# Performance work log

Hardware: AMD Instinct MI355X
Metric: run time of the kernel (lower is better)

Reference implementation:

```python
import jax, jax.numpy as jnp
import numpy as np

B, C, H, W = 4, 256, 48, 48
HEADS, DH = 8, 32
INNER = HEADS * DH
HID = 128  # max(16, INNER//2)
SCALE = DH ** -0.5
EPS = 1e-6


def setup_inputs() -> dict:
    key = jax.random.key(0)
    ks = jax.random.split(key, 32)
    s = 0.02
    inp = {
        'x': jax.random.normal(ks[0], (B, C, H, W), jnp.float32),
        'rgb_input': jax.random.uniform(ks[1], (B, 3, H, W), jnp.float32),
        'wq': jax.random.normal(ks[2], (INNER, C), jnp.float32) * s,
        'bq': jnp.zeros((INNER,), jnp.float32),
        'wk': jax.random.normal(ks[3], (INNER, C), jnp.float32) * s,
        'bk': jnp.zeros((INNER,), jnp.float32),
        'wv': jax.random.normal(ks[4], (INNER, C), jnp.float32) * s,
        'bv': jnp.zeros((INNER,), jnp.float32),
        'wproj': jax.random.normal(ks[5], (C, INNER), jnp.float32) * s,
        'bproj': jnp.zeros((C,), jnp.float32),
        'c1_w': jax.random.normal(ks[6], (HID, 1, 3, 3), jnp.float32) * s,
        'c1_b': jnp.zeros((HID,), jnp.float32),
        'c2_w': jax.random.normal(ks[7], (HID, HID, 3, 3), jnp.float32) * s,
        'c2_b': jnp.zeros((HID,), jnp.float32),
        'gq_w': jax.random.normal(ks[8], (INNER, HID), jnp.float32) * s,
        'gq_b': jnp.ones((INNER,), jnp.float32),
        'bqf_w': jax.random.normal(ks[9], (INNER, HID), jnp.float32) * s,
        'bqf_b': jnp.zeros((INNER,), jnp.float32),
        'gk_w': jax.random.normal(ks[10], (INNER, HID), jnp.float32) * s,
        'gk_b': jnp.ones((INNER,), jnp.float32),
        'bkf_w': jax.random.normal(ks[11], (INNER, HID), jnp.float32) * s,
        'bkf_b': jnp.zeros((INNER,), jnp.float32),
        'gv_w': jax.random.normal(ks[12], (INNER, HID), jnp.float32) * s,
        'gv_b': jnp.ones((INNER,), jnp.float32),
        'bvf_w': jax.random.normal(ks[13], (INNER, HID), jnp.float32) * s,
        'bvf_b': jnp.zeros((INNER,), jnp.float32),
        'alpha': jnp.float32(0.1),
    }
    return inp


def _conv3(x, w, b):
    y = jax.lax.conv_general_dilated(x, w, (1, 1), 'SAME',
                                     dimension_numbers=('NCHW', 'OIHW', 'NCHW'))
    return y + b[None, :, None, None]


def _rgb_to_luma(rgb):
    y = 0.299 * rgb[:, 0:1] + 0.587 * rgb[:, 1:2] + 0.114 * rgb[:, 2:3]
    y_min = jnp.min(y, axis=(2, 3), keepdims=True)
    y_max = jnp.max(y, axis=(2, 3), keepdims=True)
    return (y - y_min) / (y_max - y_min + EPS)


def reference(x, rgb_input, wq, bq, wk, bk, wv, bv, wproj, bproj,
              c1_w, c1_b, c2_w, c2_b,
              gq_w, gq_b, bqf_w, bqf_b, gk_w, gk_b, bkf_w, bkf_b,
              gv_w, gv_b, bvf_w, bvf_b, alpha):
    Bx, Cx, Hx, Wx = x.shape
    N = Hx * Wx
    luma = _rgb_to_luma(rgb_input)  # [B,1,H,W]

    # LumaCond trunk + FiLM params (1x1 convs then global spatial mean)
    h = jax.nn.relu(_conv3(luma, c1_w, c1_b))
    h = jax.nn.relu(_conv3(h, c2_w, c2_b))
    hm = h.mean(axis=(2, 3))  # [B,HID] (mean commutes with 1x1 conv)

    def film_params(gw, gb, bw, bb):
        g = hm @ gw.T + gb  # [B, INNER]
        bta = hm @ bw.T + bb
        return (g.reshape(Bx, HEADS, DH, 1), bta.reshape(Bx, HEADS, DH, 1))

    gq, fbq = film_params(gq_w, gq_b, bqf_w, bqf_b)
    gk, fbk = film_params(gk_w, gk_b, bkf_w, bkf_b)
    gv, fbv = film_params(gv_w, gv_b, bvf_w, bvf_b)

    def proj_film(w, b, g, bta):
        t = jnp.einsum('bchw,oc->bohw', x, w) + b[None, :, None, None]
        t = t.reshape(Bx, HEADS, DH, N)
        return g * t + bta  # [B,heads,dh,N]

    q = proj_film(wq, bq, gq, fbq)
    k = proj_film(wk, bk, gk, fbk)
    v = proj_film(wv, bv, gv, fbv)

    logits = jnp.einsum('bhdn,bhdm->bhnm', q, k) * SCALE  # [B,heads,N,N]

    # luma bias: avg-pooled inverse luma, mean-centered per image
    invL = 1.0 - luma
    invL = jax.lax.reduce_window(invL, 0.0, jax.lax.add,
                                 (1, 1, 3, 3), (1, 1, 1, 1), 'SAME') / 9.0
    invL = invL.reshape(Bx, N)
    invL = invL - invL.mean(axis=-1, keepdims=True)
    logits = logits + alpha * invL[:, None, None, :]

    attn = jax.nn.softmax(logits, axis=-1)
    out = jnp.einsum('bhnm,bhdm->bhdn', attn, v)  # [B,heads,dh,N]
    out = out.reshape(Bx, INNER, Hx, Wx)
    return jnp.einsum('bchw,oc->bohw', out, wproj) + bproj[None, :, None, None]
```

## Files before the change

### kernel.cpp

```cpp
#include <hip/hip_runtime.h>


#define NSP 2304
#define WID 48

typedef __attribute__((ext_vector_type(4))) float  fvec4;
typedef __attribute__((ext_vector_type(2))) unsigned int uvec2;
typedef __attribute__((ext_vector_type(4))) unsigned int uvec4;
typedef __attribute__((ext_vector_type(8))) short  short8;
typedef __attribute__((ext_vector_type(4))) float  f32x4;

__device__ inline unsigned short f2bf(float f){
  unsigned int u = __builtin_bit_cast(unsigned int, f);
  u += 0x7fffu + ((u >> 16) & 1u);
  return (unsigned short)(u >> 16);
}
__device__ inline unsigned pack2bf(float a, float b){
#if __has_builtin(__builtin_amdgcn_cvt_pk_bf16_f32)
  typedef __attribute__((ext_vector_type(2))) __bf16 bf16x2;
  bf16x2 r = __builtin_amdgcn_cvt_pk_bf16_f32(a, b);
  return __builtin_bit_cast(unsigned, r);
#else
  return (unsigned)f2bf(a) | ((unsigned)f2bf(b) << 16);
#endif
}

__global__ __launch_bounds__(256) void k_prep(const float* __restrict__ c2w,
    const float* __restrict__ wq, const float* __restrict__ wk, const float* __restrict__ wv_,
    const float* __restrict__ wproj, const float* __restrict__ x,
    const float* __restrict__ rgb, const float* __restrict__ alphaP,
    unsigned short* __restrict__ wtb, unsigned short* __restrict__ wqkvb,
    unsigned short* __restrict__ wprojb, unsigned short* __restrict__ xt,
    float* __restrict__ luma_n, float* __restrict__ bias_a,
    float* __restrict__ hm_sum, unsigned short* __restrict__ h1p){
  __shared__ __align__(16) float sm[5120];
  int bx = blockIdx.x, t = threadIdx.x;
  if (bx < 4){
    int b = bx;
    float* ly  = sm;
    float* ll  = sm + NSP;
    float* red = sm + 2*NSP;
    float* red2= sm + 2*NSP + 256;
    {
      const uvec4 z = {0u,0u,0u,0u};
      for (int j = t; j < 196*16; j += 256){
        int cell = j >> 4, q = j & 15;
        int r, c;
        if (cell < 50)      { r = 0;           c = cell; }
        else if (cell < 100){ r = 49;          c = cell - 50; }
        else if (cell < 148){ r = cell - 99;   c = 0; }
        else                { r = cell - 147;  c = 49; }
        *(uvec4*)(h1p + ((size_t)(b*2500 + r*50 + c))*128 + q*8) = z;
      }
    }
    const float* rp = rgb + b*3*NSP;
    float lmin = 1e30f, lmax = -1e30f;
    for (int i = t; i < NSP; i += 256){
      float y = 0.299f*rp[i] + 0.587f*rp[NSP+i] + 0.114f*rp[2*NSP+i];
      ly[i] = y; lmin = fminf(lmin, y); lmax = fmaxf(lmax, y);
    }
    red[t] = lmin; red2[t] = lmax;
    __syncthreads();
    for (int s = 128; s > 0; s >>= 1){
      if (t < s){ red[t] = fminf(red[t], red[t+s]); red2[t] = fmaxf(red2[t], red2[t+s]); }
      __syncthreads();
    }
    float mn = red[0], mx = red2[0];
    float inv = 1.0f / (mx - mn + 1e-6f);
    for (int i = t; i < NSP; i += 256){
      float v = (ly[i] - mn) * inv;
      ll[i] = v;
      luma_n[b*NSP + i] = v;
    }
    if (t < 128) hm_sum[b*128 + t] = 0.f;
    __syncthreads();
    float pr[9]; float psum = 0.f;
    #pragma unroll
    for (int ii = 0; ii < 9; ++ii){
      int n = t + 256*ii;
      int row = n / WID, col = n - row*WID;
      float s2 = 0.f;
      #pragma unroll
      for (int dy = -1; dy <= 1; ++dy)
        #pragma unroll
        for (int dx = -1; dx <= 1; ++dx){
          int r2 = row+dy, c2 = col+dx;
          if (r2 >= 0 && r2 < WID && c2 >= 0 && c2 < WID) s2 += 1.0f - ll[r2*WID + c2];
        }
      pr[ii] = s2 * (1.f/9.f);
      psum += pr[ii];
    }
    __syncthreads();
    red[t] = psum;
    __syncthreads();
    for (int s = 128; s > 0; s >>= 1){
      if (t < s) red[t] += red[t+s];
      __syncthreads();
    }
    float mean = red[0] * (1.f/(float)NSP);
    float alpha = alphaP[0] * 1.4426950408889634f;
    #pragma unroll
    for (int ii = 0; ii < 9; ++ii){
      int n = t + 256*ii;
      bias_a[b*NSP + n] = alpha * (pr[ii] - mean);
    }
  } else if (bx < 1604){
    int idx = (bx - 4)*256 + t;
    if (idx < 147456){
      int ic = idx & 127, rem = idx >> 7;
      int oc = rem & 127, tap = rem >> 7;
      wtb[idx] = f2bf(c2w[(oc*128 + ic)*9 + tap]);
    } else if (idx < 344064){
      int j = idx - 147456;
      int mat = j >> 16, oc_ = j & 65535;
      const float* src = (mat == 0) ? wq : (mat == 1) ? wk : wv_;
      wqkvb[j] = f2bf(src[oc_]);
    } else {
      int j = idx - 344064;
      wprojb[j] = f2bf(wproj[j]);
    }
  } else {
    int j = bx - 1604;
    int nt = j % 36, cc = (j / 36) & 3, b = j / 144;
    unsigned short* tb = (unsigned short*)sm;
    int cl0 = t >> 4;
    int nl0 = (t & 15) * 4;
    #pragma unroll
    for (int ps_ = 0; ps_ < 4; ++ps_){
      int cl = cl0 + ps_*16;
      fvec4 v = *(const fvec4*)(x + ((size_t)(b*256 + cc*64 + cl))*NSP + nt*64 + nl0);
      #pragma unroll
      for (int i = 0; i < 4; ++i) tb[(nl0+i)*72 + cl] = f2bf(v[i]);
    }
    __syncthreads();
    int nl = t >> 2, cg = (t & 3) * 16;
    uvec4 u0 = *(const uvec4*)&tb[nl*72 + cg];
    uvec4 u1 = *(const uvec4*)&tb[nl*72 + cg + 8];
    unsigned short* dst = xt + ((size_t)(b*NSP + nt*64 + nl))*256 + cc*64 + cg;
    *(uvec4*)dst = u0;
    *(uvec4*)(dst + 8) = u1;
  }
}

__global__ void k2_conv1(const float* __restrict__ luma_n, const float* __restrict__ c1w,
                         const float* __restrict__ c1b, unsigned short* __restrict__ h1p){
  int nt = blockIdx.x, ocg = blockIdx.y, b = blockIdx.z, t = threadIdx.x;
  __shared__ float wsm[32*9];
  __shared__ float bsm[32];
  for (int i = t; i < 288; i += 256) wsm[i] = c1w[ocg*288 + i];
  if (t < 32) bsm[t] = c1b[ocg*32 + t];
  __syncthreads();
  int n = nt*256 + t;
  int row = n / WID, col = n - row*WID;
  const float* lp = luma_n + b*NSP;
  float lv[9];
  int k = 0;
  #pragma unroll
  for (int dy = -1; dy <= 1; ++dy)
    #pragma unroll
    for (int dx = -1; dx <= 1; ++dx, ++k){
      int r2 = row+dy, c2 = col+dx;
      lv[k] = (r2 >= 0 && r2 < WID && c2 >= 0 && c2 < WID) ? lp[r2*WID + c2] : 0.f;
    }
  unsigned int packed[16];
  #pragma unroll
  for (int oc2 = 0; oc2 < 16; ++oc2){
    float a0 = bsm[oc2*2], a1 = bsm[oc2*2+1];
    #pragma unroll
    for (int q = 0; q < 9; ++q){
      a0 += wsm[(oc2*2)*9 + q] * lv[q];
      a1 += wsm[(oc2*2+1)*9 + q] * lv[q];
    }
    packed[oc2] = pack2bf(fmaxf(a0, 0.f), fmaxf(a1, 0.f));
  }
  unsigned short* dst = h1p + ((size_t)(b*2500 + (row+1)*50 + (col+1)))*128 + ocg*32;
  #pragma unroll
  for (int q4 = 0; q4 < 4; ++q4)
    *(uvec4*)(dst + q4*8) = *(uvec4*)&packed[q4*4];
}

__global__ __launch_bounds__(256) void k3_conv2(const unsigned short* __restrict__ h1p,
    const unsigned short* __restrict__ wtb, const float* __restrict__ c2b,
    float* __restrict__ hm_sum){
  int row = blockIdx.x, mh = blockIdx.y, b = blockIdx.z;
  int t = threadIdx.x, wv = t >> 6, lane = t & 63;
  int lq = lane >> 4, lc = lane & 15;
  int ocb = mh*64 + wv*16;
  const f32x4 z4 = {0.f, 0.f, 0.f, 0.f};
  f32x4 C[3] = {z4, z4, z4};
  const unsigned short* hbase = h1p + (size_t)b*2500*128;
  #pragma unroll
  for (int tap = 0; tap < 9; ++tap){
    int dy = tap/3 - 1, dx = tap%3 - 1;
    const unsigned short* wrow = wtb + (tap*128 + ocb + lc)*128 + lq*8;
    const unsigned short* hrow = hbase + ((row+dy+1)*50 + (dx+1) + lc)*128 + lq*8;
    #pragma unroll
    for (int kc = 0; kc < 4; ++kc){
      short8 aW = *(const short8*)(wrow + kc*32);
      #pragma unroll
      for (int ntp = 0; ntp < 3; ++ntp){
        short8 bH = *(const short8*)(hrow + ntp*16*128 + kc*32);
        C[ntp] = __builtin_amdgcn_mfma_f32_16x16x32_bf16(aW, bH, C[ntp], 0, 0, 0);
      }
    }
  }
  float s[4];
  #pragma unroll
  for (int r = 0; r < 4; ++r){
    float bias = c2b[ocb + lq*4 + r];
    float v = 0.f;
    #pragma unroll
    for (int ntp = 0; ntp < 3; ++ntp) v += fmaxf(C[ntp][r] + bias, 0.f);
    v += __shfl_xor(v, 1, 64);
    v += __shfl_xor(v, 2, 64);
    v += __shfl_xor(v, 4, 64);
    v += __shfl_xor(v, 8, 64);
    s[r] = v;
  }
  if (lc == 0){
    #pragma unroll
    for (int r = 0; r < 4; ++r)
      atomicAdd(&hm_sum[b*128 + ocb + lq*4 + r], s[r]);
  }
}

__global__ void k4_film(const float* __restrict__ hm_sum,
  const float* w0, const float* b0, const float* w1, const float* b1,
  const float* w2, const float* b2, const float* w3, const float* b3,
  const float* w4, const float* b4, const float* w5, const float* b5,
  float* __restrict__ film){
  __shared__ float hs[128];
  int bb = blockIdx.x & 3, m6 = blockIdx.x >> 2, t = threadIdx.x;
  if (t < 128) hs[t] = hm_sum[bb*128 + t] * (1.f/(float)NSP);
  __syncthreads();
  const float* wm[6] = {w0,w1,w2,w3,w4,w5};
  const float* bm[6] = {b0,b1,b2,b3,b4,b5};
  const float* w = wm[m6];
  int o = t;
  float a = bm[m6][o];
  for (int h2 = 0; h2 < 128; ++h2) a += hs[h2] * w[o*128 + h2];
  film[blockIdx.x*256 + t] = a;
}

__global__ __launch_bounds__(256) void k5_qkv(const unsigned short* __restrict__ xt,
    const unsigned short* __restrict__ wqkvb,
    const float* __restrict__ bq, const float* __restrict__ bk, const float* __restrict__ bv,
    const float* __restrict__ film,
    unsigned short* __restrict__ q_t, unsigned short* __restrict__ k_t,
    unsigned short* __restrict__ v_b){
  int nt = blockIdx.x, ot = blockIdx.y, b = blockIdx.z;
  int t = threadIdx.x, wv = t >> 6, lane = t & 63;
  int lq = lane >> 4, lc = lane & 15;
  int p = ot >> 1;
  int omb = (ot & 1)*128 + wv*32;
  const f32x4 z4 = {0.f, 0.f, 0.f, 0.f};
  f32x4 acc[2][4];
  #pragma unroll
  for (int oh = 0; oh < 2; ++oh)
    #pragma unroll
    for (int nq = 0; nq < 4; ++nq) acc[oh][nq] = z4;

  const unsigned short* wbp = wqkvb + p*65536 + (omb + lc)*256 + lq*8;
  const unsigned short* xbp = xt + ((size_t)(b*NSP + nt*64 + lc))*256 + lq*8;

  short8 aW0[2], aW1[2], bX0[4], bX1[4];
  auto loadW = [&](short8 (&W)[2], int kc){
    #pragma unroll
    for (int oh = 0; oh < 2; ++oh) W[oh] = *(const short8*)(wbp + oh*16*256 + kc*32);
  };
  auto loadX = [&](short8 (&X)[4], int kc){
    #pragma unroll
    for (int nq = 0; nq < 4; ++nq) X[nq] = *(const short8*)(xbp + (size_t)nq*16*256 + kc*32);
  };
  auto mm = [&](short8 (&W)[2], short8 (&X)[4]){
    #pragma unroll
    for (int oh = 0; oh < 2; ++oh)
      #pragma unroll
      for (int nq = 0; nq < 4; ++nq)
        acc[oh][nq] = __builtin_amdgcn_mfma_f32_16x16x32_bf16(W[oh], X[nq], acc[oh][nq], 0, 0, 0);
  };
  loadW(aW0, 0); loadX(bX0, 0);
  for (int kc2 = 0; kc2 < 4; ++kc2){
    loadW(aW1, kc2*2+1); loadX(bX1, kc2*2+1);
    mm(aW0, bX0);
    int kn = (kc2*2+2) & 7;
    loadW(aW0, kn); loadX(bX0, kn);
    mm(aW1, bX1);
  }

  const float* bvec = (p == 0) ? bq : (p == 1) ? bk : bv;
  int hq = omb >> 5;
  unsigned short* qk = (p == 0) ? q_t : k_t;
  #pragma unroll
  for (int oh = 0; oh < 2; ++oh){
    fvec4 g4 = *(const fvec4*)(film + (2*p*4 + b)*256 + omb + oh*16 + lq*4);
    fvec4 t4 = *(const fvec4*)(film + ((2*p+1)*4 + b)*256 + omb + oh*16 + lq*4);
    fvec4 z4b = *(const fvec4*)(bvec + omb + oh*16 + lq*4);
    #pragma unroll
    for (int nq = 0; nq < 4; ++nq){
      int n = nt*64 + nq*16 + lc;
      float v0 = g4[0]*(acc[oh][nq][0] + z4b[0]) + t4[0];
      float v1 = g4[1]*(acc[oh][nq][1] + z4b[1]) + t4[1];
      float v2 = g4[2]*(acc[oh][nq][2] + z4b[2]) + t4[2];
      float v3 = g4[3]*(acc[oh][nq][3] + z4b[3]) + t4[3];
      if (p == 0){
        const float sc = 0.17677669529663687f * 1.4426950408889634f;
        v0 *= sc; v1 *= sc; v2 *= sc; v3 *= sc;
      }
      if (p < 2){
        uvec2 u;
        u.x = pack2bf(v0, v1);
        u.y = pack2bf(v2, v3);
        *(uvec2*)(qk + ((size_t)((b*8 + hq)*NSP + n))*32 + oh*16 + lq*4) = u;
      } else {
        int om = omb + oh*16 + lq*4;
        v_b[((size_t)(b*256 + om + 0))*NSP + n] = f2bf(v0);
        v_b[((size_t)(b*256 + om + 1))*NSP + n] = f2bf(v1);
        v_b[((size_t)(b*256 + om + 2))*NSP + n] = f2bf(v2);
        v_b[((size_t)(b*256 + om + 3))*NSP + n] = f2bf(v3);
      }
    }
  }
}

__global__ __launch_bounds__(256, 4) void k6_attn(const unsigned short* __restrict__ q_t,
    const unsigned short* __restrict__ k_t, const unsigned short* __restrict__ v_b,
    const float* __restrict__ bias_a,
    unsigned short* __restrict__ o0, unsigned short* __restrict__ o1,
    unsigned short* __restrict__ o2,
    float* __restrict__ l0, float* __restrict__ l1, float* __restrict__ l2){
  int bx = blockIdx.x, h = blockIdx.y, b = blockIdx.z;
  int qblk = bx / 3, s = bx - qblk*3;
  unsigned short* op = (s == 0) ? o0 : (s == 1) ? o1 : o2;
  float* lp = (s == 0) ? l0 : (s == 1) ? l1 : l2;
  int t = threadIdx.x, wv = t >> 6, lane = t & 63;
  int lq = lane >> 4, lc = lane & 15;
  int bh = b*8 + h;
  int nb0 = qblk*128 + wv*32;
  const f32x4 z4 = {0.f, 0.f, 0.f, 0.f};
  int ms = s*768;

  __shared__ unsigned short Kb[2][64*32];
  __shared__ unsigned short Vb[2][32*64];
  __shared__ float ps[4][512];

  const unsigned short* kg = k_t + ((size_t)bh*NSP + ms + (t>>2))*32 + (t&3)*8;
  const unsigned short* vg = v_b + ((size_t)(b*256 + h*32 + (t>>3)))*NSP + ms + (t&7)*8;
  int krow = t >> 2;
  unsigned short* kw = &Kb[0][krow*32 + (((t&3) ^ ((krow>>1)&3))*8)];
  int vrow = t >> 3;
  unsigned short* vw = &Vb[0][vrow*64 + (((t&7) ^ (vrow&7))*8)];

  int kcol = (lq ^ ((lc>>1)&3))*8;
  int sxm = ((lc&7)<<2) | (((lc>>3)&1)<<1);
  int wbase = lc*32;

  const float* brow = bias_a + b*NSP + ms;
  fvec4 c0r[4];
  #pragma unroll
  for (int g = 0; g < 4; ++g) c0r[g] = *(const fvec4*)(brow + g*16 + lq*4);

  short8 aQ[2];
  #pragma unroll
  for (int qf = 0; qf < 2; ++qf)
    aQ[qf] = *(const short8*)(q_t + ((size_t)(bh*NSP + nb0 + qf*16 + lc))*32 + lq*8);

  uvec4 gKr = *(const uvec4*)kg;
  uvec4 gVr = *(const uvec4*)vg;

  const uvec4 onesu = {0x3F803F80u, 0x3F803F80u, 0x3F803F80u, 0x3F803F80u};
  const short8 aOnes = __builtin_bit_cast(short8, onesu);

  f32x4 O[2][2]; f32x4 Ol[2];
  #pragma unroll
  for (int qf = 0; qf < 2; ++qf){
    Ol[qf] = z4; O[qf][0] = z4; O[qf][1] = z4;
  }
  float* myps = ps[wv];

  for (int it = 0; it < 12; ++it){
    int buf = it & 1;
    *(uvec4*)(kw + buf*2048) = gKr;
    *(uvec4*)(vw + buf*2048) = gVr;
    __syncthreads();
    if (it < 11){
      gKr = *(const uvec4*)(kg + (it+1)*2048);
      gVr = *(const uvec4*)(vg + (it+1)*64);
    }
    const unsigned short* kb = Kb[buf];
    const unsigned short* vb = Vb[buf];
    short8 aK[4], aV[2][2];
    #pragma unroll
    for (int g = 0; g < 4; ++g)
      aK[g] = *(const short8*)(kb + (g*16 + lc)*32 + kcol);
    #pragma unroll
    for (int dhg = 0; dhg < 2; ++dhg)
      #pragma unroll
      for (int mh = 0; mh < 2; ++mh)
        aV[dhg][mh] = *(const short8*)(vb + (dhg*16 + lc)*64 + (((mh*4 + lq) ^ (lc&7))*8));
    #pragma unroll
    for (int qf = 0; qf < 2; ++qf){
      #pragma unroll
      for (int g = 0; g < 4; ++g){
        f32x4 S = __builtin_amdgcn_mfma_f32_16x16x32_bf16(aK[g], aQ[qf], c0r[g], 0, 0, 0);
        uvec2 w2;
        w2.x = pack2bf(__builtin_amdgcn_exp2f(S[0]), __builtin_amdgcn_exp2f(S[1]));
        w2.y = pack2bf(__builtin_amdgcn_exp2f(S[2]), __builtin_amdgcn_exp2f(S[3]));
        *(uvec2*)&myps[wbase + ((g*8 + lq*2) ^ sxm)] = w2;
      }
      if (qf == 1 && it < 11){
        #pragma unroll
        for (int g = 0; g < 4; ++g)
          c0r[g] = *(const fvec4*)(brow + (it+1)*64 + g*16 + lq*4);
      }
      __builtin_amdgcn_s_setprio(1);
      #pragma unroll
      for (int mh = 0; mh < 2; ++mh){
        int d0 = (mh*16 + lq*4) ^ sxm;
        uvec2 lo = *(const uvec2*)&myps[wbase + d0];
        uvec2 hi = *(const uvec2*)&myps[wbase + (d0 ^ 2)];
        uvec4 up; up.x = lo.x; up.y = lo.y; up.z = hi.x; up.w = hi.y;
        short8 bP = __builtin_bit_cast(short8, up);
        Ol[qf] = __builtin_amdgcn_mfma_f32_16x16x32_bf16(aOnes, bP, Ol[qf], 0, 0, 0);
        #pragma unroll
        for (int dhg = 0; dhg < 2; ++dhg)
          O[qf][dhg] = __builtin_amdgcn_mfma_f32_16x16x32_bf16(aV[dhg][mh], bP, O[qf][dhg], 0, 0, 0);
      }
      __builtin_amdgcn_s_setprio(0);
    }
  }
  #pragma unroll
  for (int qf = 0; qf < 2; ++qf){
    int nidx = nb0 + qf*16 + lc;
    if (lq == 0) lp[b*NSP + nidx] = Ol[qf][0];
    #pragma unroll
    for (int dh = 0; dh < 2; ++dh){
      uvec2 u;
      u.x = pack2bf(O[qf][dh][0], O[qf][dh][1]);
      u.y = pack2bf(O[qf][dh][2], O[qf][dh][3]);
      *(uvec2*)(op + ((size_t)(b*NSP + nidx))*256 + h*32 + dh*16 + lq*4) = u;
    }
  }
}

__global__ __launch_bounds__(256) void k7_proj(const unsigned short* __restrict__ a0,
    const unsigned short* __restrict__ a1, const unsigned short* __restrict__ a2,
    const float* __restrict__ l0p, const float* __restrict__ l1p,
    const float* __restrict__ l2p, const unsigned short* __restrict__ wprojb,
    const float* __restrict__ bproj, float* __restrict__ out){
  int nt = blockIdx.x, ct = blockIdx.y, b = blockIdx.z;
  int t = threadIdx.x, wv = t >> 6, lane = t & 63;
  int lq = lane >> 4, lc = lane & 15;
  __shared__ float rls[32];
  if (t < 32) rls[t] = 1.0f / (l0p[b*NSP + nt*32 + t] + l1p[b*NSP + nt*32 + t]
                               + l2p[b*NSP + nt*32 + t]);
  __syncthreads();
  int cb = ct*128 + wv*32;
  const f32x4 z4 = {0.f, 0.f, 0.f, 0.f};
  f32x4 acc[2][2];
  #pragma unroll
  for (int ch = 0; ch < 2; ++ch)
    #pragma unroll
    for (int nq = 0; nq < 2; ++nq) acc[ch][nq] = z4;

  const unsigned short* wpp = wprojb + (cb + lc)*256 + lq*8;
  const unsigned short* a0p = a0 + ((size_t)(b*NSP + nt*32 + lc))*256 + lq*8;
  const unsigned short* a1p = a1 + ((size_t)(b*NSP + nt*32 + lc))*256 + lq*8;
  const unsigned short* a2p = a2 + ((size_t)(b*NSP + nt*32 + lc))*256 + lq*8;

  short8 W0[2], W1[2], B0[3][2], B1[3][2];
  auto loadS = [&](short8 (&W)[2], short8 (&B)[3][2], int kc){
    #pragma unroll
    for (int ch = 0; ch < 2; ++ch) W[ch] = *(const short8*)(wpp + ch*16*256 + kc*32);
    #pragma unroll
    for (int nq = 0; nq < 2; ++nq){
      B[0][nq] = *(const short8*)(a0p + (size_t)nq*16*256 + kc*32);
      B[1][nq] = *(const short8*)(a1p + (size_t)nq*16*256 + kc*32);
      B[2][nq] = *(const short8*)(a2p + (size_t)nq*16*256 + kc*32);
    }
  };
  auto mmS = [&](short8 (&W)[2], short8 (&B)[3][2]){
    #pragma unroll
    for (int src = 0; src < 3; ++src)
      #pragma unroll
      for (int ch = 0; ch < 2; ++ch)
        #pragma unroll
        for (int nq = 0; nq < 2; ++nq)
          acc[ch][nq] = __builtin_amdgcn_mfma_f32_16x16x32_bf16(W[ch], B[src][nq], acc[ch][nq], 0, 0, 0);
  };
  loadS(W0, B0, 0);
  for (int kc2 = 0; kc2 < 4; ++kc2){
    loadS(W1, B1, kc2*2+1);
    mmS(W0, B0);
    int kn = (kc2*2+2) & 7;
    loadS(W0, B0, kn);
    mmS(W1, B1);
  }

  #pragma unroll
  for (int ch = 0; ch < 2; ++ch){
    #pragma unroll
    for (int nq = 0; nq < 2; ++nq){
      int n = nt*32 + nq*16 + lc;
      float rl = rls[nq*16 + lc];
      #pragma unroll
      for (int r = 0; r < 4; ++r){
        int c = cb + ch*16 + lq*4 + r;
        out[((size_t)(b*256 + c))*NSP + n] = acc[ch][nq][r]*rl + bproj[c];
      }
    }
  }
}

extern "C" void kernel_launch(void* const* d_in, const int* in_sizes, int n_in,
                              void* d_out, int out_size, void* d_ws, size_t ws_size,
                              hipStream_t stream) {
  const float* x     = (const float*)d_in[0];
  const float* rgb   = (const float*)d_in[1];
  const float* wq    = (const float*)d_in[2];
  const float* bq    = (const float*)d_in[3];
  const float* wk    = (const float*)d_in[4];
  const float* bk    = (const float*)d_in[5];
  const float* wv    = (const float*)d_in[6];
  const float* bv    = (const float*)d_in[7];
  const float* wproj = (const float*)d_in[8];
  const float* bproj = (const float*)d_in[9];
  const float* c1w   = (const float*)d_in[10];
  const float* c1b   = (const float*)d_in[11];
  const float* c2w   = (const float*)d_in[12];
  const float* c2b   = (const float*)d_in[13];
  const float* gq_w  = (const float*)d_in[14];
  const float* gq_b  = (const float*)d_in[15];
  const float* bqf_w = (const float*)d_in[16];
  const float* bqf_b = (const float*)d_in[17];
  const float* gk_w  = (const float*)d_in[18];
  const float* gk_b  = (const float*)d_in[19];
  const float* bkf_w = (const float*)d_in[20];
  const float* bkf_b = (const float*)d_in[21];
  const float* gv_w  = (const float*)d_in[22];
  const float* gv_b  = (const float*)d_in[23];
  const float* bvf_w = (const float*)d_in[24];
  const float* bvf_b = (const float*)d_in[25];
  const float* alphaP= (const float*)d_in[26];

  char* w = (char*)d_ws;
  float* luma_n = (float*)w;            w += 4*NSP*4;
  float* bias_a = (float*)w;            w += 4*NSP*4;
  float* hm_sum = (float*)w;            w += 512*4;
  float* film   = (float*)w;            w += 6*4*256*4;
  unsigned short* h1p = (unsigned short*)w; w += 4*2500*128*2;
  unsigned short* wtb = (unsigned short*)w; w += 9*128*128*2;
  unsigned short* wqkvb = (unsigned short*)w; w += 3*256*256*2;
  unsigned short* wprojb = (unsigned short*)w; w += 256*256*2;
  unsigned short* xt  = (unsigned short*)w; w += (size_t)4*NSP*256*2;
  unsigned short* q_t = (unsigned short*)w; w += (size_t)4*8*NSP*32*2;
  unsigned short* k_t = (unsigned short*)w; w += (size_t)4*8*NSP*32*2;
  unsigned short* v_b = (unsigned short*)w; w += (size_t)4*256*NSP*2;
  unsigned short* o_part0 = (unsigned short*)w; w += (size_t)4*NSP*256*2;
  unsigned short* o_part1 = (unsigned short*)w; w += (size_t)4*NSP*256*2;
  float* l_part0 = (float*)w;           w += 4*NSP*4;
  float* l_part1 = (float*)w;           w += 4*NSP*4;
  float* l_part2 = (float*)w;           w += 4*NSP*4;
  unsigned short* o_part2 = xt;

  k_prep  <<<2180, 256, 0, stream>>>(c2w, wq, wk, wv, wproj, x, rgb, alphaP,
                                     wtb, wqkvb, wprojb, xt,
                                     luma_n, bias_a, hm_sum, h1p);
  k2_conv1<<<dim3(9,4,4), 256, 0, stream>>>(luma_n, c1w, c1b, h1p);
  k3_conv2<<<dim3(48,2,4), 256, 0, stream>>>(h1p, wtb, c2b, hm_sum);
  k4_film <<<24, 256, 0, stream>>>(hm_sum, gq_w, gq_b, bqf_w, bqf_b,
                                   gk_w, gk_b, bkf_w, bkf_b,
                                   gv_w, gv_b, bvf_w, bvf_b, film);
  k5_qkv  <<<dim3(36,6,4), 256, 0, stream>>>(xt, wqkvb, bq, bk, bv, film,
                                             q_t, k_t, v_b);
  k6_attn <<<dim3(54,8,4), 256, 0, stream>>>(q_t, k_t, v_b, bias_a,
                                             o_part0, o_part1, o_part2,
                                             l_part0, l_part1, l_part2);
  k7_proj <<<dim3(72,2,4), 256, 0, stream>>>(o_part0, o_part1, o_part2,
                                             l_part0, l_part1, l_part2,
                                             wprojb, bproj, (float*)d_out);
}
```

Before: 261.1 us.

## Fuse conv1 into prep kernel and FiLM projection into QKV kernel

Computes the first 1-channel conv directly inside the luma blocks of the prep kernel from shared-memory luma, and has each QKV block compute its needed FiLM gamma/beta rows from the pooled hidden vector. This removes two kernel launches and the luma_n and film round-trips through global memory. In exchange, only 4 blocks now do the whole conv1 (128 channels per pixel, serialized), which may lengthen the prep kernel's critical path. Every QKV block also redundantly recomputes a 128-wide matvec before its main work.

```diff
diff --git a/kernel.cpp b/kernel.cpp
--- a/kernel.cpp
+++ b/kernel.cpp
@@ -29,10 +29,11 @@
     const float* __restrict__ wq, const float* __restrict__ wk, const float* __restrict__ wv_,
     const float* __restrict__ wproj, const float* __restrict__ x,
     const float* __restrict__ rgb, const float* __restrict__ alphaP,
+    const float* __restrict__ c1w, const float* __restrict__ c1b,
     unsigned short* __restrict__ wtb, unsigned short* __restrict__ wqkvb,
     unsigned short* __restrict__ wprojb, unsigned short* __restrict__ xt,
-    float* __restrict__ luma_n, float* __restrict__ bias_a,
-    float* __restrict__ hm_sum, unsigned short* __restrict__ h1p){
+    float* __restrict__ bias_a, float* __restrict__ hm_sum,
+    unsigned short* __restrict__ h1p){
   __shared__ __align__(16) float sm[5120];
   int bx = blockIdx.x, t = threadIdx.x;
   if (bx < 4){
@@ -41,6 +42,8 @@
     float* ll  = sm + NSP;
     float* red = sm + 2*NSP;
     float* red2= sm + 2*NSP + 256;
+    float* wsm = sm;
+    float* bsm = sm + 1152;
     {
       const uvec4 z = {0u,0u,0u,0u};
       for (int j = t; j < 196*16; j += 256){
@@ -67,13 +70,12 @@
     }
     float mn = red[0], mx = red2[0];
     float inv = 1.0f / (mx - mn + 1e-6f);
-    for (int i = t; i < NSP; i += 256){
-      float v = (ly[i] - mn) * inv;
-      ll[i] = v;
-      luma_n[b*NSP + i] = v;
-    }
+    for (int i = t; i < NSP; i += 256)
+      ll[i] = (ly[i] - mn) * inv;
     if (t < 128) hm_sum[b*128 + t] = 0.f;
     __syncthreads();
+    for (int i = t; i < 1152; i += 256) wsm[i] = c1w[i];
+    if (t < 128) bsm[t] = c1b[t];
     float pr[9]; float psum = 0.f;
     #pragma unroll
     for (int ii = 0; ii < 9; ++ii){
@@ -103,6 +105,39 @@
     for (int ii = 0; ii < 9; ++ii){
       int n = t + 256*ii;
       bias_a[b*NSP + n] = alpha * (pr[ii] - mean);
+    }
+    #pragma unroll
+    for (int ii = 0; ii < 9; ++ii){
+      int n = t + 256*ii;
+      int row = n / WID, col = n - row*WID;
+      float lv[9];
+      int k = 0;
+      #pragma unroll
+      for (int dy = -1; dy <= 1; ++dy)
+        #pragma unroll
+        for (int dx = -1; dx <= 1; ++dx, ++k){
+          int r2 = row+dy, c2 = col+dx;
+          lv[k] = (r2 >= 0 && r2 < WID && c2 >= 0 && c2 < WID) ? ll[r2*WID + c2] : 0.f;
+        }
+      unsigned short* dst = h1p + ((size_t)(b*2500 + (row+1)*50 + (col+1)))*128;
+      #pragma unroll
+      for (int ocg = 0; ocg < 4; ++ocg){
+        unsigned int packed[16];
+        #pragma unroll
+        for (int oc2 = 0; oc2 < 16; ++oc2){
+          int oc = ocg*32 + oc2*2;
+          float a0 = bsm[oc], a1 = bsm[oc+1];
+          #pragma unroll
+          for (int q = 0; q < 9; ++q){
+            a0 += wsm[oc*9 + q] * lv[q];
+            a1 += wsm[(oc+1)*9 + q] * lv[q];
+          }
+          packed[oc2] = pack2bf(fmaxf(a0, 0.f), fmaxf(a1, 0.f));
+        }
+        #pragma unroll
+        for (int q4 = 0; q4 < 4; ++q4)
+          *(uvec4*)(dst + ocg*32 + q4*8) = *(uvec4*)&packed[q4*4];
+      }
     }
   } else if (bx < 1604){
     int idx = (bx - 4)*256 + t;
@@ -142,43 +177,6 @@
   }
 }
 
-__global__ void k2_conv1(const float* __restrict__ luma_n, const float* __restrict__ c1w,
-                         const float* __restrict__ c1b, unsigned short* __restrict__ h1p){
-  int nt = blockIdx.x, ocg = blockIdx.y, b = blockIdx.z, t = threadIdx.x;
-  __shared__ float wsm[32*9];
-  __shared__ float bsm[32];
-  for (int i = t; i < 288; i += 256) wsm[i] = c1w[ocg*288 + i];
-  if (t < 32) bsm[t] = c1b[ocg*32 + t];
-  __syncthreads();
-  int n = nt*256 + t;
-  int row = n / WID, col = n - row*WID;
-  const float* lp = luma_n + b*NSP;
-  float lv[9];
-  int k = 0;
-  #pragma unroll
-  for (int dy = -1; dy <= 1; ++dy)
-    #pragma unroll
-    for (int dx = -1; dx <= 1; ++dx, ++k){
-      int r2 = row+dy, c2 = col+dx;
-      lv[k] = (r2 >= 0 && r2 < WID && c2 >= 0 && c2 < WID) ? lp[r2*WID + c2] : 0.f;
-    }
-  unsigned int packed[16];
-  #pragma unroll
-  for (int oc2 = 0; oc2 < 16; ++oc2){
-    float a0 = bsm[oc2*2], a1 = bsm[oc2*2+1];
-    #pragma unroll
-    for (int q = 0; q < 9; ++q){
-      a0 += wsm[(oc2*2)*9 + q] * lv[q];
-      a1 += wsm[(oc2*2+1)*9 + q] * lv[q];
-    }
-    packed[oc2] = pack2bf(fmaxf(a0, 0.f), fmaxf(a1, 0.f));
-  }
-  unsigned short* dst = h1p + ((size_t)(b*2500 + (row+1)*50 + (col+1)))*128 + ocg*32;
-  #pragma unroll
-  for (int q4 = 0; q4 < 4; ++q4)
-    *(uvec4*)(dst + q4*8) = *(uvec4*)&packed[q4*4];
-}
-
 __global__ __launch_bounds__(256) void k3_conv2(const unsigned short* __restrict__ h1p,
     const unsigned short* __restrict__ wtb, const float* __restrict__ c2b,
     float* __restrict__ hm_sum){
@@ -224,35 +222,48 @@
   }
 }
 
-__global__ void k4_film(const float* __restrict__ hm_sum,
-  const float* w0, const float* b0, const float* w1, const float* b1,
-  const float* w2, const float* b2, const float* w3, const float* b3,
-  const float* w4, const float* b4, const float* w5, const float* b5,
-  float* __restrict__ film){
-  __shared__ float hs[128];
-  int bb = blockIdx.x & 3, m6 = blockIdx.x >> 2, t = threadIdx.x;
-  if (t < 128) hs[t] = hm_sum[bb*128 + t] * (1.f/(float)NSP);
-  __syncthreads();
-  const float* wm[6] = {w0,w1,w2,w3,w4,w5};
-  const float* bm[6] = {b0,b1,b2,b3,b4,b5};
-  const float* w = wm[m6];
-  int o = t;
-  float a = bm[m6][o];
-  for (int h2 = 0; h2 < 128; ++h2) a += hs[h2] * w[o*128 + h2];
-  film[blockIdx.x*256 + t] = a;
-}
-
 __global__ __launch_bounds__(256) void k5_qkv(const unsigned short* __restrict__ xt,
     const unsigned short* __restrict__ wqkvb,
     const float* __restrict__ bq, const float* __restrict__ bk, const float* __restrict__ bv,
-    const float* __restrict__ film,
+    const float* __restrict__ hm_sum,
+    const float* __restrict__ gq_w, const float* __restrict__ gq_b,
+    const float* __restrict__ bqf_w, const float* __restrict__ bqf_b,
+    const float* __restrict__ gk_w, const float* __restrict__ gk_b,
+    const float* __restrict__ bkf_w, const float* __restrict__ bkf_b,
+    const float* __restrict__ gv_w, const float* __restrict__ gv_b,
+    const float* __restrict__ bvf_w, const float* __restrict__ bvf_b,
     unsigned short* __restrict__ q_t, unsigned short* __restrict__ k_t,
     unsigned short* __restrict__ v_b){
   int nt = blockIdx.x, ot = blockIdx.y, b = blockIdx.z;
   int t = threadIdx.x, wv = t >> 6, lane = t & 63;
   int lq = lane >> 4, lc = lane & 15;
   int p = ot >> 1;
-  int omb = (ot & 1)*128 + wv*32;
+  int half = ot & 1;
+  int omb = half*128 + wv*32;
+
+  __shared__ __align__(16) float hs[128];
+  __shared__ __align__(16) float flm[256];
+  if (t < 128) hs[t] = hm_sum[b*128 + t] * (1.f/(float)NSP);
+  __syncthreads();
+  {
+    const float* gw  = (p == 0) ? gq_w  : (p == 1) ? gk_w  : gv_w;
+    const float* gbv = (p == 0) ? gq_b  : (p == 1) ? gk_b  : gv_b;
+    const float* bw  = (p == 0) ? bqf_w : (p == 1) ? bkf_w : bvf_w;
+    const float* bbv = (p == 0) ? bqf_b : (p == 1) ? bkf_b : bvf_b;
+    int type = t >> 7;
+    int o = half*128 + (t & 127);
+    const float* wrow = (type ? bw : gw) + o*128;
+    float a = type ? bbv[o] : gbv[o];
+    #pragma unroll 8
+    for (int i = 0; i < 32; ++i){
+      fvec4 w4 = *(const fvec4*)(wrow + i*4);
+      fvec4 h4 = *(const fvec4*)(&hs[i*4]);
+      a += w4[0]*h4[0] + w4[1]*h4[1] + w4[2]*h4[2] + w4[3]*h4[3];
+    }
+    flm[t] = a;
+  }
+  __syncthreads();
+
   const f32x4 z4 = {0.f, 0.f, 0.f, 0.f};
   f32x4 acc[2][4];
   #pragma unroll
@@ -293,8 +304,9 @@
   unsigned short* qk = (p == 0) ? q_t : k_t;
   #pragma unroll
   for (int oh = 0; oh < 2; ++oh){
-    fvec4 g4 = *(const fvec4*)(film + (2*p*4 + b)*256 + omb + oh*16 + lq*4);
-    fvec4 t4 = *(const fvec4*)(film + ((2*p+1)*4 + b)*256 + omb + oh*16 + lq*4);
+    int fo = wv*32 + oh*16 + lq*4;
+    fvec4 g4 = *(const fvec4*)&flm[fo];
+    fvec4 t4 = *(const fvec4*)&flm[128 + fo];
     fvec4 z4b = *(const fvec4*)(bvec + omb + oh*16 + lq*4);
     #pragma unroll
     for (int nq = 0; nq < 4; ++nq){
@@ -544,10 +556,8 @@
   const float* alphaP= (const float*)d_in[26];
 
   char* w = (char*)d_ws;
-  float* luma_n = (float*)w;            w += 4*NSP*4;
   float* bias_a = (float*)w;            w += 4*NSP*4;
   float* hm_sum = (float*)w;            w += 512*4;
-  float* film   = (float*)w;            w += 6*4*256*4;
   unsigned short* h1p = (unsigned short*)w; w += 4*2500*128*2;
   unsigned short* wtb = (unsigned short*)w; w += 9*128*128*2;
   unsigned short* wqkvb = (unsigned short*)w; w += 3*256*256*2;
@@ -564,14 +574,13 @@
   unsigned short* o_part2 = xt;
 
   k_prep  <<<2180, 256, 0, stream>>>(c2w, wq, wk, wv, wproj, x, rgb, alphaP,
-                                     wtb, wqkvb, wprojb, xt,
-                                     luma_n, bias_a, hm_sum, h1p);
-  k2_conv1<<<dim3(9,4,4), 256, 0, stream>>>(luma_n, c1w, c1b, h1p);
+                                     c1w, c1b, wtb, wqkvb, wprojb, xt,
+                                     bias_a, hm_sum, h1p);
   k3_conv2<<<dim3(48,2,4), 256, 0, stream>>>(h1p, wtb, c2b, hm_sum);
-  k4_film <<<24, 256, 0, stream>>>(hm_sum, gq_w, gq_b, bqf_w, bqf_b,
-                                   gk_w, gk_b, bkf_w, bkf_b,
-                                   gv_w, gv_b, bvf_w, bvf_b, film);
-  k5_qkv  <<<dim3(36,6,4), 256, 0, stream>>>(xt, wqkvb, bq, bk, bv, film,
+  k5_qkv  <<<dim3(36,6,4), 256, 0, stream>>>(xt, wqkvb, bq, bk, bv, hm_sum,
+                                             gq_w, gq_b, bqf_w, bqf_b,
+                                             gk_w, gk_b, bkf_w, bkf_b,
+                                             gv_w, gv_b, bvf_w, bvf_b,
                                              q_t, k_t, v_b);
   k6_attn <<<dim3(54,8,4), 256, 0, stream>>>(q_t, k_t, v_b, bias_a,
                                              o_part0, o_part1, o_part2,
```

After: 599.7 us. +129.7%, slower.
